# Kernel tuning notes

Hardware: AMD Instinct MI355X
Metric: run time of the kernel (lower is better)

## Reference

```python
import jax, jax.numpy as jnp
import numpy as np

IN_CAPS = 512
NUM_CAPS = 64
DIM_CAPS = 16
NUM_ROUTING = 3
BETA = 1.0  # config['Model']['temperature']
IN_DIM = 768
Q_N = 512
EPS = 1e-8


def squash(s):
    # capsule squash along last dim
    n2 = jnp.sum(s * s, axis=-1, keepdims=True)
    return (n2 / (1.0 + n2)) * s / jnp.sqrt(n2 + EPS)


def pearsonr(x, y):
    # pearson correlation along last dim, broadcasting leading dims
    xm = x - jnp.mean(x, axis=-1, keepdims=True)
    ym = y - jnp.mean(y, axis=-1, keepdims=True)
    num = jnp.sum(xm * ym, axis=-1)
    den = jnp.sqrt(jnp.sum(xm * xm, axis=-1) * jnp.sum(ym * ym, axis=-1) + EPS)
    return num / den


def setup_inputs() -> dict:
    key = jax.random.key(0)
    k1, k2, k3, k4 = jax.random.split(key, 4)
    m = jax.random.normal(k1, (IN_CAPS, IN_DIM), dtype=jnp.float32)
    q = jax.random.normal(k2, (Q_N, IN_DIM), dtype=jnp.float32)
    W_w = jax.random.normal(k3, (IN_DIM, NUM_CAPS * DIM_CAPS), dtype=jnp.float32) * 0.02
    W_b = jax.random.normal(k4, (NUM_CAPS * DIM_CAPS,), dtype=jnp.float32) * 0.02
    return {"m": m, "q": q, "W_w": W_w, "W_b": W_b}


def reference(m, q, W_w, W_b):
    nq = q.shape[0]
    hat_m = (m @ W_w + W_b).reshape(IN_CAPS, NUM_CAPS, DIM_CAPS)          # [I,C,D]
    hat_q = (q @ W_w + W_b).reshape(nq, NUM_CAPS, DIM_CAPS)               # [Q,C,D]

    m_sg = jax.lax.stop_gradient(hat_m)                                    # detached copies used in routing
    # torch expands hat_q along in_caps but updates it uniformly -> keep broadcast dim of size 1
    q_cur = jax.lax.stop_gradient(hat_q)[:, None, :, :]                    # [Q,1,C,D]

    a = jnp.zeros((nq, IN_CAPS, NUM_CAPS), dtype=hat_m.dtype)             # routing logits
    p = jnp.tanh(pearsonr(m_sg[None], q_cur))                              # [Q,I,C]

    for _ in range(NUM_ROUTING - 1):
        d = jax.nn.softmax(a / BETA, axis=2)                               # softmax over num_caps (as in torch dim=2)
        d_sum_p = d + p                                                     # [Q,I,C]
        hat_v = jnp.einsum('qic,icd->qcd', d_sum_p, m_sg)                  # sum over in_caps
        v = squash(hat_v)                                                   # [Q,C,D]
        hat_m_cos_v = jnp.einsum('icd,qcd->qic', m_sg, v)                  # [Q,I,C]
        a = a + p * hat_m_cos_v
        q_cur = (q_cur + v[:, None]) / 2.0                                  # stays [Q,1,C,D]
        p = jnp.tanh(pearsonr(m_sg[None], q_cur))

    d = jax.nn.softmax(a / BETA, axis=2)
    d_sum_p = jax.lax.stop_gradient(d + p)                                  # detached coefficients
    hat_v = jnp.einsum('qic,icd->qcd', d_sum_p, hat_m)                      # grad flows only through hat_m
    q_prime = squash(hat_v).reshape(nq, -1)                                 # [Q, C*D]
    return q_prime
```

## Files before the change

kernel.cpp:

```cpp
#include <hip/hip_runtime.h>
#include <math.h>

#define IN_CAPS 512
#define QN      512
#define IN_DIM  768
#define NCAPS   64
#define DCAPS   16
#define CD      1024

typedef _Float16 half2_t __attribute__((ext_vector_type(2)));

#if __has_builtin(__builtin_amdgcn_rcpf)
  #define RCP(x) __builtin_amdgcn_rcpf(x)
#else
  #define RCP(x) __frcp_rn(x)
#endif

__device__ __forceinline__ float tanh_pade(float x){
  const float x2 = x*x;
  const float num = fmaf(x2, x2 + 105.0f, 945.0f);
  const float den = fmaf(x2, fmaf(x2, 15.0f, 420.0f), 945.0f);
  return x * num * RCP(den);
}

template<int CTRL>
__device__ __forceinline__ float dpp_add(float v){
  int r = __builtin_amdgcn_update_dpp(0, __float_as_int(v), CTRL, 0xF, 0xF, true);
  return v + __int_as_float(r);
}

__device__ __forceinline__ float wave_sum64_all(float v){
  v = dpp_add<0xB1>(v);
  v = dpp_add<0x4E>(v);
  v = dpp_add<0x141>(v);
  v = dpp_add<0x140>(v);
  v = dpp_add<0x142>(v);
  v = dpp_add<0x143>(v);
  return __int_as_float(__builtin_amdgcn_readlane(__float_as_int(v), 63));
}

#define LD16(dst, ptr) { const float4* _p=(const float4*)(ptr); \
  float4 _a=_p[0], _b=_p[1], _c=_p[2], _d=_p[3]; \
  dst[0]=_a.x; dst[1]=_a.y; dst[2]=_a.z; dst[3]=_a.w; \
  dst[4]=_b.x; dst[5]=_b.y; dst[6]=_b.z; dst[7]=_b.w; \
  dst[8]=_c.x; dst[9]=_c.y; dst[10]=_c.z; dst[11]=_c.w; \
  dst[12]=_d.x; dst[13]=_d.y; dst[14]=_d.z; dst[15]=_d.w; }

#define ST16(ptr, src) { float4* _p=(float4*)(ptr); \
  _p[0]=make_float4(src[0],src[1],src[2],src[3]); \
  _p[1]=make_float4(src[4],src[5],src[6],src[7]); \
  _p[2]=make_float4(src[8],src[9],src[10],src[11]); \
  _p[3]=make_float4(src[12],src[13],src[14],src[15]); }

#define LDH(dst, ptrf4) { const float4* _p=(const float4*)(ptrf4); \
  float4 _a=_p[0], _b=_p[1]; \
  dst[0]=__builtin_bit_cast(half2_t,_a.x); dst[1]=__builtin_bit_cast(half2_t,_a.y); \
  dst[2]=__builtin_bit_cast(half2_t,_a.z); dst[3]=__builtin_bit_cast(half2_t,_a.w); \
  dst[4]=__builtin_bit_cast(half2_t,_b.x); dst[5]=__builtin_bit_cast(half2_t,_b.y); \
  dst[6]=__builtin_bit_cast(half2_t,_b.z); dst[7]=__builtin_bit_cast(half2_t,_b.w); }

#define CVT16(dst, h) { \
  _Pragma("unroll") for (int _j=0;_j<8;_j++){ \
    dst[2*_j]   = (float)h[_j].x; \
    dst[2*_j+1] = (float)h[_j].y; } }

#define STH16(ptr, src) { float _tb[8]; \
  _Pragma("unroll") for (int _j=0;_j<8;_j++){ half2_t _h; _h.x=(_Float16)src[2*_j]; _h.y=(_Float16)src[2*_j+1]; _tb[_j]=__builtin_bit_cast(float,_h);} \
  float4* _p=(float4*)(ptr); \
  _p[0]=make_float4(_tb[0],_tb[1],_tb[2],_tb[3]); \
  _p[1]=make_float4(_tb[4],_tb[5],_tb[6],_tb[7]); }

#define DOT16(res, x, y) { float _e=0.f,_o=0.f; \
  _Pragma("unroll") for (int _d=0;_d<16;_d+=2){ _e = fmaf(x[_d],y[_d],_e); _o = fmaf(x[_d+1],y[_d+1],_o); } \
  res = _e+_o; }

#define ACCUM(acc, m, w) { \
  _Pragma("unroll") for (int _d=0;_d<16;_d++) acc[_d] = fmaf(w, m[_d], acc[_d]); }

#define QSTAT(qcc, s1v, qq) { \
  float qc_[16]; \
  LD16(qc_, hat + (size_t)(IN_CAPS + (qq))*CD + c*16); \
  float s_=0.f; \
  _Pragma("unroll") for (int d=0;d<16;d++) s_ += qc_[d]; \
  const float mean_ = s_*(1.0f/16.0f); \
  float n2_=0.f; \
  _Pragma("unroll") for (int d=0;d<16;d++){ qcc[d]=qc_[d]-mean_; n2_ += qcc[d]*qcc[d]; } \
  s1v = __frsqrt_rn(n2_ + 1e-12f); }

#define WDECODE() \
  const int tid = threadIdx.x; \
  const int gw  = blockIdx.x*4 + (tid >> 6); \
  const int q   = gw >> cshift; \
  const int ch  = gw & (nch-1); \
  const int c   = tid & 63;

__global__ __launch_bounds__(256) void gemm_hat(const float* __restrict__ m,
                                                const float* __restrict__ q,
                                                const float* __restrict__ Ww,
                                                float* __restrict__ hatP)
{
  __shared__ float As[16][65];
  __shared__ float Bs[16][65];
  const int tid = threadIdx.x;
  const int bm = blockIdx.y, bn = blockIdx.x, kz = blockIdx.z;
  const int tx = tid & 15, ty = tid >> 4;

  float acc[4][4];
  #pragma unroll
  for (int a=0;a<4;a++)
    #pragma unroll
    for (int b=0;b<4;b++) acc[a][b]=0.0f;

  const int r  = tid >> 2;
  const int kk = (tid & 3) << 2;
  const int row = bm*64 + r;
  const float* srcA = (row < IN_CAPS) ? (m + row*IN_DIM) : (q + (row-IN_CAPS)*IN_DIM);
  const int krow = tid >> 4;
  const int cc   = (tid & 15) << 2;

  const int kbeg = kz*(IN_DIM/4), kend = kbeg + IN_DIM/4;
  for (int k0=kbeg; k0<kend; k0+=16){
    float4 av = *(const float4*)(srcA + k0 + kk);
    As[kk+0][r]=av.x; As[kk+1][r]=av.y; As[kk+2][r]=av.z; As[kk+3][r]=av.w;
    float4 bv = *(const float4*)(Ww + (size_t)(k0+krow)*CD + bn*64 + cc);
    Bs[krow][cc+0]=bv.x; Bs[krow][cc+1]=bv.y; Bs[krow][cc+2]=bv.z; Bs[krow][cc+3]=bv.w;
    __syncthreads();
    #pragma unroll
    for (int k=0;k<16;k++){
      float a[4], b[4];
      #pragma unroll
      for (int j=0;j<4;j++) a[j] = As[k][ty*4+j];
      #pragma unroll
      for (int j=0;j<4;j++) b[j] = Bs[k][tx*4+j];
      #pragma unroll
      for (int ii=0;ii<4;ii++)
        #pragma unroll
        for (int jj=0;jj<4;jj++) acc[ii][jj] += a[ii]*b[jj];
    }
    __syncthreads();
  }
  float* dst = hatP + (size_t)kz*1048576;
  const int col0 = bn*64 + tx*4;
  #pragma unroll
  for (int ii=0;ii<4;ii++){
    const int orow = bm*64 + ty*4 + ii;
    #pragma unroll
    for (int jj=0;jj<4;jj++) dst[(size_t)orow*CD + col0 + jj] = acc[ii][jj];
  }
}

__global__ __launch_bounds__(256) void finish_stats_kernel(const float4* __restrict__ hatP4,
                                                           const float* __restrict__ Wb,
                                                           float4* __restrict__ hat4,
                                                           _Float16* __restrict__ hatH,
                                                           float2* __restrict__ rs,
                                                           float* __restrict__ s1g,
                                                           _Float16* __restrict__ qccH)
{
  __shared__ float rowbuf[1024];
  const int row = blockIdx.x;
  const int t = threadIdx.x;
  const size_t o = (size_t)row*256 + t;
  float4 a = hatP4[o];
  float4 b = hatP4[o + 262144];
  float4 cx = hatP4[o + 524288];
  float4 d = hatP4[o + 786432];
  const float4 wb = *(const float4*)(Wb + t*4);
  float4 r;
  r.x = a.x+b.x+cx.x+d.x+wb.x;
  r.y = a.y+b.y+cx.y+d.y+wb.y;
  r.z = a.z+b.z+cx.z+d.z+wb.z;
  r.w = a.w+b.w+cx.w+d.w+wb.w;
  hat4[o] = r;
  if (row < IN_CAPS){
    half2_t h0, h1;
    h0.x=(_Float16)r.x; h0.y=(_Float16)r.y;
    h1.x=(_Float16)r.z; h1.y=(_Float16)r.w;
    *(float2*)(hatH + (size_t)row*CD + t*4) =
      make_float2(__builtin_bit_cast(float,h0), __builtin_bit_cast(float,h1));
  }
  rowbuf[t*4+0]=r.x; rowbuf[t*4+1]=r.y; rowbuf[t*4+2]=r.z; rowbuf[t*4+3]=r.w;
  __syncthreads();
  if (t < 64){
    const int c = t;
    float v[16];
    #pragma unroll
    for (int dd=0;dd<16;dd++) v[dd] = rowbuf[c*16+dd];
    float s=0.f;
    #pragma unroll
    for (int dd=0;dd<16;dd++) s += v[dd];
    const float mean = s*(1.0f/16.0f);
    float n2=0.f;
    #pragma unroll
    for (int dd=0;dd<16;dd++){ float x=v[dd]-mean; n2+=x*x; }
    if (row < IN_CAPS){
      rs[row*64+c] = make_float2(__frsqrt_rn(n2 + 1e-12f), s);
    } else {
      const int qr = row - IN_CAPS;
      s1g[qr*64 + c] = __frsqrt_rn(n2 + 1e-12f);
      float tbuf[8];
      #pragma unroll
      for (int j=0;j<8;j++){
        half2_t h; h.x=(_Float16)(v[2*j]-mean); h.y=(_Float16)(v[2*j+1]-mean);
        tbuf[j] = __builtin_bit_cast(float, h);
      }
      float4* dst = (float4*)(qccH + (size_t)qr*CD + c*16);
      dst[0] = make_float4(tbuf[0],tbuf[1],tbuf[2],tbuf[3]);
      dst[1] = make_float4(tbuf[4],tbuf[5],tbuf[6],tbuf[7]);
    }
  }
}

template<bool CACHED>
__global__ __launch_bounds__(256) void pass1_kernel(const float4* __restrict__ hatH4,
                                                    const float4* __restrict__ qccH4,
                                                    const float* __restrict__ s1g,
                                                    const float2* __restrict__ rs_g,
                                                    _Float16* __restrict__ part,
                                                    _Float16* __restrict__ n1h,
                                                    int ilen, int nch, int cshift)
{
  WDECODE();
  float qcc1[16];
  {
    half2_t qh[8];
    LDH(qh, qccH4 + (size_t)q*128 + c*2);
    CVT16(qcc1, qh);
  }
  const float s1 = s1g[q*64+c];

  float acc[16];
  #pragma unroll
  for (int d=0;d<16;d++) acc[d]=0.f;

  const int i0 = ch*ilen;
  const float4* mp = hatH4 + (size_t)i0*128 + c*2;
  const float2* rp = rs_g + i0*64 + c;
  size_t idx = ((size_t)q*512 + i0)*64 + c;
  for (int i=0;i<ilen;i+=2, mp+=256, rp+=128, idx+=128){
    half2_t ha[8], hb[8];
    LDH(ha, mp); LDH(hb, mp+128);
    float ma[16], mb[16];
    CVT16(ma, ha); CVT16(mb, hb);
    const float ra = rp[0].x, rb = rp[64].x;
    float nA, nB;
    DOT16(nA, ma, qcc1);
    DOT16(nB, mb, qcc1);
    if (CACHED){
      n1h[idx]    = (_Float16)nA;
      n1h[idx+64] = (_Float16)nB;
    }
    const float wA = 0.015625f + tanh_pade(nA*ra*s1);
    const float wB = 0.015625f + tanh_pade(nB*rb*s1);
    ACCUM(acc, ma, wA);
    ACCUM(acc, mb, wB);
  }
  STH16(part + (((size_t)(q<<cshift) + ch)*64 + c)*16, acc);
}

__global__ __launch_bounds__(256) void reduce1_kernel(const float* __restrict__ hat,
                                                      const _Float16* __restrict__ part,
                                                      float* __restrict__ v1g,
                                                      float2* __restrict__ aux1,
                                                      int nchunk)
{
  const int tid = threadIdx.x;
  const int q = blockIdx.x*4 + (tid>>6), c = tid & 63;
  float hv[16];
  #pragma unroll
  for (int d=0;d<16;d++) hv[d]=0.f;
  const _Float16* pp = part + ((size_t)q*nchunk*64 + c)*16;
  for (int ch=0; ch<nchunk; ch++, pp += 1024){
    half2_t th[8]; LDH(th, pp);
    float t[16]; CVT16(t, th);
    #pragma unroll
    for (int d=0;d<16;d++) hv[d]+=t[d];
  }
  float n2=0.f;
  #pragma unroll
  for (int d=0;d<16;d++) n2 += hv[d]*hv[d];
  const float sc = n2 / ((1.0f+n2)*sqrtf(n2+1e-8f));
  float v1[16]; float sv=0.f;
  #pragma unroll
  for (int d=0;d<16;d++){ v1[d]=hv[d]*sc; sv+=v1[d]; }
  ST16(v1g + ((size_t)q*64 + c)*16, v1);
  float qc[16]; LD16(qc, hat + (size_t)(IN_CAPS+q)*CD + c*16);
  float s=0.f, ss=0.f;
  #pragma unroll
  for (int d=0;d<16;d++){ const float t2 = 0.5f*(qc[d]+v1[d]); s+=t2; ss+=t2*t2; }
  const float mean = s*(1.0f/16.0f);
  aux1[q*64+c] = make_float2(__frsqrt_rn(ss - 16.0f*mean*mean + 1e-12f), sv*(1.0f/16.0f));
}

template<bool CACHED>
__global__ __launch_bounds__(256) void pass2_kernel(const float4* __restrict__ hatH4,
                                                    const float* __restrict__ hat,
                                                    const float2* __restrict__ rs_g,
                                                    const float* __restrict__ s1g,
                                                    const float* __restrict__ v1g,
                                                    const float2* __restrict__ aux1,
                                                    _Float16* __restrict__ part,
                                                    _Float16* __restrict__ n1h,
                                                    float* __restrict__ c2f,
                                                    int ilen, int nch, int cshift)
{
  WDECODE();
  float qcc1[16]; float s1;
  if (CACHED){
    s1 = s1g[q*64+c];
  } else {
    QSTAT(qcc1, s1, q);
  }
  float v1[16];
  LD16(v1, v1g + ((size_t)q*64 + c)*16);
  const float2 a1 = aux1[q*64+c];
  const float s2 = a1.x, mv1 = a1.y;

  float acc[16];
  #pragma unroll
  for (int d=0;d<16;d++) acc[d]=0.f;

  const int i0 = ch*ilen;
  const float4* mp = hatH4 + (size_t)i0*128 + c*2;
  const float2* rp = rs_g + i0*64 + c;
  size_t idx = ((size_t)q*512 + i0)*64 + c;
  for (int i=0;i<ilen;i+=2, mp+=256, rp+=128, idx+=128){
    half2_t ha[8], hb[8];
    LDH(ha, mp); LDH(hb, mp+128);
    float ma[16], mb[16];
    CVT16(ma, ha); CVT16(mb, hb);
    const float2 ra = rp[0], rb = rp[64];
    float n1A, n1B, cvA, cvB;
    if (CACHED){
      n1A = (float)n1h[idx];
      n1B = (float)n1h[idx+64];
    } else {
      DOT16(n1A, ma, qcc1);
      DOT16(n1B, mb, qcc1);
    }
    DOT16(cvA, ma, v1);
    DOT16(cvB, mb, v1);
    const float p1A = tanh_pade(n1A*ra.x*s1);
    const float n2A = 0.5f*(n1A + cvA - mv1*ra.y);
    const float p2A = tanh_pade(n2A*ra.x*s2);
    const float p1B = tanh_pade(n1B*rb.x*s1);
    const float n2B = 0.5f*(n1B + cvB - mv1*rb.y);
    const float p2B = tanh_pade(n2B*rb.x*s2);
    const float l1A = p1A*cvA;
    const float l1B = p1B*cvB;
    if (CACHED){
      half2_t cA; cA.x = (_Float16)l1A; cA.y = (_Float16)p2A;
      half2_t cB; cB.x = (_Float16)l1B; cB.y = (_Float16)p2B;
      c2f[idx]    = __builtin_bit_cast(float, cA);
      c2f[idx+64] = __builtin_bit_cast(float, cB);
      n1h[idx]    = (_Float16)n2A;
      n1h[idx+64] = (_Float16)n2B;
    }
    const float eA = __expf(l1A);
    const float eB = __expf(l1B);
    const float SA = wave_sum64_all(eA);
    const float SB = wave_sum64_all(eB);
    const float wA = eA*RCP(SA) + p2A;
    const float wB = eB*RCP(SB) + p2B;
    ACCUM(acc, ma, wA);
    ACCUM(acc, mb, wB);
  }
  STH16(part + (((size_t)(q<<cshift) + ch)*64 + c)*16, acc);
}

__global__ __launch_bounds__(256) void reduce2_kernel(const float* __restrict__ hat,
                                                      const _Float16* __restrict__ part,
                                                      const float* __restrict__ v1g,
                                                      float* __restrict__ v2g,
                                                      float2* __restrict__ aux2,
                                                      int nchunk)
{
  const int tid = threadIdx.x;
  const int q = blockIdx.x*4 + (tid>>6), c = tid & 63;
  float hv[16];
  #pragma unroll
  for (int d=0;d<16;d++) hv[d]=0.f;
  const _Float16* pp = part + ((size_t)q*nchunk*64 + c)*16;
  for (int ch=0; ch<nchunk; ch++, pp += 1024){
    half2_t th[8]; LDH(th, pp);
    float t[16]; CVT16(t, th);
    #pragma unroll
    for (int d=0;d<16;d++) hv[d]+=t[d];
  }
  float n2=0.f;
  #pragma unroll
  for (int d=0;d<16;d++) n2 += hv[d]*hv[d];
  const float sc = n2 / ((1.0f+n2)*sqrtf(n2+1e-8f));
  float v2[16]; float sv=0.f;
  #pragma unroll
  for (int d=0;d<16;d++){ v2[d]=hv[d]*sc; sv+=v2[d]; }
  ST16(v2g + ((size_t)q*64 + c)*16, v2);
  float qc[16];  LD16(qc, hat + (size_t)(IN_CAPS+q)*CD + c*16);
  float v1[16];  LD16(v1, v1g + ((size_t)q*64 + c)*16);
  float s=0.f, ss=0.f;
  #pragma unroll
  for (int d=0;d<16;d++){
    const float t3 = 0.25f*qc[d] + 0.25f*v1[d] + 0.5f*v2[d];
    s+=t3; ss+=t3*t3;
  }
  const float mean = s*(1.0f/16.0f);
  aux2[q*64+c] = make_float2(__frsqrt_rn(ss - 16.0f*mean*mean + 1e-12f), sv*(1.0f/16.0f));
}

template<bool CACHED>
__global__ __launch_bounds__(256) void pass3_kernel(const float4* __restrict__ hatH4,
                                                    const float* __restrict__ hat,
                                                    const float2* __restrict__ rs_g,
                                                    const float* __restrict__ v1g,
                                                    const float* __restrict__ v2g,
                                                    const float2* __restrict__ aux1,
                                                    const float2* __restrict__ aux2,
                                                    _Float16* __restrict__ part,
                                                    const _Float16* __restrict__ n1h,
                                                    const float* __restrict__ c2f,
                                                    int ilen, int nch, int cshift)
{
  WDECODE();
  float v2[16];
  LD16(v2, v2g + ((size_t)q*64 + c)*16);
  const float2 a2 = aux2[q*64+c];
  const float s3 = a2.x, mv2 = a2.y;

  float qcc1[16]; float s1=0.f, s2=0.f, mv1=0.f;
  float v1[16];
  if (!CACHED){
    QSTAT(qcc1, s1, q);
    LD16(v1, v1g + ((size_t)q*64 + c)*16);
    const float2 a1 = aux1[q*64+c];
    s2 = a1.x; mv1 = a1.y;
  }

  float acc[16];
  #pragma unroll
  for (int d=0;d<16;d++) acc[d]=0.f;

  const int i0 = ch*ilen;
  const float4* mp = hatH4 + (size_t)i0*128 + c*2;
  const float2* rp = rs_g + i0*64 + c;
  size_t idx = ((size_t)q*512 + i0)*64 + c;
  for (int i=0;i<ilen;i+=2, mp+=256, rp+=128, idx+=128){
    half2_t ha[8], hb[8];
    LDH(ha, mp); LDH(hb, mp+128);
    float ma[16], mb[16];
    CVT16(ma, ha); CVT16(mb, hb);
    const float2 ra = rp[0], rb = rp[64];
    float cwA, cwB;
    DOT16(cwA, ma, v2);
    DOT16(cwB, mb, v2);
    float l1A, p2A, n2A, l1B, p2B, n2B;
    if (CACHED){
      half2_t cA = __builtin_bit_cast(half2_t, c2f[idx]);
      half2_t cB = __builtin_bit_cast(half2_t, c2f[idx+64]);
      l1A = (float)cA.x; p2A = (float)cA.y;
      l1B = (float)cB.x; p2B = (float)cB.y;
      n2A = (float)n1h[idx];
      n2B = (float)n1h[idx+64];
    } else {
      float n1A, cvA, n1B, cvB;
      DOT16(n1A, ma, qcc1); DOT16(cvA, ma, v1);
      DOT16(n1B, mb, qcc1); DOT16(cvB, mb, v1);
      const float p1A = tanh_pade(n1A*ra.x*s1);
      n2A = 0.5f*(n1A + cvA - mv1*ra.y);
      p2A = tanh_pade(n2A*ra.x*s2);
      l1A = p1A*cvA;
      const float p1B = tanh_pade(n1B*rb.x*s1);
      n2B = 0.5f*(n1B + cvB - mv1*rb.y);
      p2B = tanh_pade(n2B*rb.x*s2);
      l1B = p1B*cvB;
    }
    const float n3A = 0.5f*(n2A + cwA - mv2*ra.y);
    const float p3A = tanh_pade(n3A*ra.x*s3);
    const float n3B = 0.5f*(n2B + cwB - mv2*rb.y);
    const float p3B = tanh_pade(n3B*rb.x*s3);
    const float eA = __expf(fmaf(p2A, cwA, l1A));
    const float eB = __expf(fmaf(p2B, cwB, l1B));
    const float SA = wave_sum64_all(eA);
    const float SB = wave_sum64_all(eB);
    const float wA = eA*RCP(SA) + p3A;
    const float wB = eB*RCP(SB) + p3B;
    ACCUM(acc, ma, wA);
    ACCUM(acc, mb, wB);
  }
  STH16(part + (((size_t)(q<<cshift) + ch)*64 + c)*16, acc);
}

__global__ __launch_bounds__(256) void reduce3_kernel(const _Float16* __restrict__ part,
                                                      float* __restrict__ out,
                                                      int nchunk)
{
  const int tid = threadIdx.x;
  const int q = blockIdx.x*4 + (tid>>6), c = tid & 63;
  float hv[16];
  #pragma unroll
  for (int d=0;d<16;d++) hv[d]=0.f;
  const _Float16* pp = part + ((size_t)q*nchunk*64 + c)*16;
  for (int ch=0; ch<nchunk; ch++, pp += 1024){
    half2_t th[8]; LDH(th, pp);
    float t[16]; CVT16(t, th);
    #pragma unroll
    for (int d=0;d<16;d++) hv[d]+=t[d];
  }
  float n2=0.f;
  #pragma unroll
  for (int d=0;d<16;d++) n2 += hv[d]*hv[d];
  const float sc = n2 / ((1.0f+n2)*sqrtf(n2+1e-8f));
  float o[16];
  #pragma unroll
  for (int d=0;d<16;d++) o[d] = hv[d]*sc;
  ST16(out + (size_t)q*CD + c*16, o);
}

extern "C" void kernel_launch(void* const* d_in, const int* in_sizes, int n_in,
                              void* d_out, int out_size, void* d_ws, size_t ws_size,
                              hipStream_t stream)
{
  const float* m  = (const float*)d_in[0];
  const float* q  = (const float*)d_in[1];
  const float* Ww = (const float*)d_in[2];
  const float* Wb = (const float*)d_in[3];
  float* out = (float*)d_out;

  char* ws = (char*)d_ws;
  float*    hat  = (float*)   (ws + 0);
  float2*   rs   = (float2*)  (ws + 4194304);
  _Float16* hatH = (_Float16*)(ws + 4456448);
  float*    s1g  = (float*)   (ws + 5505024);
  _Float16* qccH = (_Float16*)(ws + 5636096);
  float*    v1g  = (float*)   (ws + 6684672);
  float*    v2g  = (float*)   (ws + 8781824);
  float2*   aux1 = (float2*)  (ws + 10878976);
  float2*   aux2 = (float2*)  (ws + 11141120);
  const size_t base = 11403264ull;
  const size_t CACHE_BYTES = 33554432ull + 67108864ull;

  auto spanOf = [](int nc){ size_t s = (size_t)nc*1048576ull; return s < 16777216ull ? 16777216ull : s; };

  int nchunk = 16, cshift = 4;
  bool cached;
  {
    int nc = 16, cs = 4;
    while (nc > 1 && base + spanOf(nc) + CACHE_BYTES > ws_size){ nc >>= 1; cs--; }
    cached = (base + spanOf(nc) + CACHE_BYTES <= ws_size);
    if (cached){ nchunk = nc; cshift = cs; }
    else {
      while (nchunk > 1 && base + spanOf(nchunk) > ws_size){ nchunk >>= 1; cshift--; }
    }
  }
  const size_t span = spanOf(nchunk);
  _Float16* part = (_Float16*)(ws + base);
  float*    hatP = (float*)   (ws + base);
  _Float16* n1h  = (_Float16*)(ws + base + span);
  float*    c2f  = (float*)   (ws + base + span + 33554432ull);

  const int ilen = 512 / nchunk;
  const int pblocks = (QN*nchunk)/4;

  dim3 g0(16,16,4);
  gemm_hat<<<g0, 256, 0, stream>>>(m, q, Ww, hatP);
  finish_stats_kernel<<<1024, 256, 0, stream>>>((const float4*)hatP, Wb, (float4*)hat, hatH, rs, s1g, qccH);
  if (cached){
    pass1_kernel<true><<<pblocks, 256, 0, stream>>>((const float4*)hatH, (const float4*)qccH, s1g, rs, part, n1h, ilen, nchunk, cshift);
    reduce1_kernel<<<128, 256, 0, stream>>>(hat, part, v1g, aux1, nchunk);
    pass2_kernel<true><<<pblocks, 256, 0, stream>>>((const float4*)hatH, hat, rs, s1g, v1g, aux1, part, n1h, c2f, ilen, nchunk, cshift);
    reduce2_kernel<<<128, 256, 0, stream>>>(hat, part, v1g, v2g, aux2, nchunk);
    pass3_kernel<true><<<pblocks, 256, 0, stream>>>((const float4*)hatH, hat, rs, v1g, v2g, aux1, aux2, part, n1h, c2f, ilen, nchunk, cshift);
    reduce3_kernel<<<128, 256, 0, stream>>>(part, out, nchunk);
  } else {
    pass1_kernel<false><<<pblocks, 256, 0, stream>>>((const float4*)hatH, (const float4*)qccH, s1g, rs, part, n1h, ilen, nchunk, cshift);
    reduce1_kernel<<<128, 256, 0, stream>>>(hat, part, v1g, aux1, nchunk);
    pass2_kernel<false><<<pblocks, 256, 0, stream>>>((const float4*)hatH, hat, rs, s1g, v1g, aux1, part, n1h, c2f, ilen, nchunk, cshift);
    reduce2_kernel<<<128, 256, 0, stream>>>(hat, part, v1g, v2g, aux2, nchunk);
    pass3_kernel<false><<<pblocks, 256, 0, stream>>>((const float4*)hatH, hat, rs, v1g, v2g, aux1, aux2, part, n1h, c2f, ilen, nchunk, cshift);
    reduce3_kernel<<<128, 256, 0, stream>>>(part, out, nchunk);
  }
}
```

Measured before the change: 196.8 us.

## Process two queries per wave in routing passes to reuse capsule loads

Adds pass1/2/3 variants where each wave handles a pair of queries, so every loaded hat_m row (fp16) and its stats are reused for two queries. This halves the grid size and the global reads of the in-capsule tensor in the cached path. In exchange it doubles the live registers (two accumulators and two query vectors), which may lower occupancy, and halves the number of blocks available for parallelism.

```diff
diff --git a/kernel.cpp b/kernel.cpp
--- a/kernel.cpp
+++ b/kernel.cpp
@@ -92,6 +92,14 @@
   const int gw  = blockIdx.x*4 + (tid >> 6); \
   const int q   = gw >> cshift; \
   const int ch  = gw & (nch-1); \
+  const int c   = tid & 63;
+
+#define WDECODE2() \
+  const int tid = threadIdx.x; \
+  const int gw  = blockIdx.x*4 + (tid >> 6); \
+  const int qp  = gw >> cshift; \
+  const int ch  = gw & (nch-1); \
+  const int q0  = qp*2, q1 = q0+1; \
   const int c   = tid & 63;
 
 __global__ __launch_bounds__(256) void gemm_hat(const float* __restrict__ m,
@@ -210,6 +218,177 @@
     }
   }
 }
+
+
+__global__ __launch_bounds__(256) void pass1_q2(const float4* __restrict__ hatH4,
+                                                const float4* __restrict__ qccH4,
+                                                const float* __restrict__ s1g,
+                                                const float2* __restrict__ rs_g,
+                                                _Float16* __restrict__ part,
+                                                _Float16* __restrict__ n1h,
+                                                int ilen, int nch, int cshift)
+{
+  WDECODE2();
+  float qccA[16], qccB[16];
+  { half2_t qh[8]; LDH(qh, qccH4 + (size_t)q0*128 + c*2); CVT16(qccA, qh); }
+  { half2_t qh[8]; LDH(qh, qccH4 + (size_t)q1*128 + c*2); CVT16(qccB, qh); }
+  const float s1A = s1g[q0*64+c], s1B = s1g[q1*64+c];
+
+  float accA[16], accB[16];
+  #pragma unroll
+  for (int d=0;d<16;d++){ accA[d]=0.f; accB[d]=0.f; }
+
+  const int i0 = ch*ilen;
+  const float4* mp = hatH4 + (size_t)i0*128 + c*2;
+  const float2* rp = rs_g + i0*64 + c;
+  size_t idxA = ((size_t)q0*512 + i0)*64 + c;
+  size_t idxB = idxA + 32768;
+  for (int i=0;i<ilen;i++, mp+=128, rp+=64, idxA+=64, idxB+=64){
+    half2_t h[8];
+    LDH(h, mp);
+    float mr[16];
+    CVT16(mr, h);
+    const float rn = rp->x;
+    float nA, nB;
+    DOT16(nA, mr, qccA);
+    DOT16(nB, mr, qccB);
+    n1h[idxA] = (_Float16)nA;
+    n1h[idxB] = (_Float16)nB;
+    const float wA = 0.015625f + tanh_pade(nA*rn*s1A);
+    const float wB = 0.015625f + tanh_pade(nB*rn*s1B);
+    ACCUM(accA, mr, wA);
+    ACCUM(accB, mr, wB);
+  }
+  STH16(part + (((size_t)(q0<<cshift) + ch)*64 + c)*16, accA);
+  STH16(part + (((size_t)(q1<<cshift) + ch)*64 + c)*16, accB);
+}
+
+__global__ __launch_bounds__(256) void pass2_q2(const float4* __restrict__ hatH4,
+                                                const float2* __restrict__ rs_g,
+                                                const float* __restrict__ s1g,
+                                                const float* __restrict__ v1g,
+                                                const float2* __restrict__ aux1,
+                                                _Float16* __restrict__ part,
+                                                _Float16* __restrict__ n1h,
+                                                float* __restrict__ c2f,
+                                                int ilen, int nch, int cshift)
+{
+  WDECODE2();
+  const float s1A = s1g[q0*64+c], s1B = s1g[q1*64+c];
+  float v1A[16], v1B[16];
+  LD16(v1A, v1g + ((size_t)q0*64 + c)*16);
+  LD16(v1B, v1g + ((size_t)q1*64 + c)*16);
+  const float2 a1A = aux1[q0*64+c];
+  const float2 a1B = aux1[q1*64+c];
+  const float s2A = a1A.x, mv1A = a1A.y;
+  const float s2B = a1B.x, mv1B = a1B.y;
+
+  float accA[16], accB[16];
+  #pragma unroll
+  for (int d=0;d<16;d++){ accA[d]=0.f; accB[d]=0.f; }
+
+  const int i0 = ch*ilen;
+  const float4* mp = hatH4 + (size_t)i0*128 + c*2;
+  const float2* rp = rs_g + i0*64 + c;
+  size_t idxA = ((size_t)q0*512 + i0)*64 + c;
+  size_t idxB = idxA + 32768;
+  for (int i=0;i<ilen;i++, mp+=128, rp+=64, idxA+=64, idxB+=64){
+    half2_t h[8];
+    LDH(h, mp);
+    float mr[16];
+    CVT16(mr, h);
+    const float2 rn = *rp;
+    const float n1A = (float)n1h[idxA];
+    const float n1B = (float)n1h[idxB];
+    float cvA, cvB;
+    DOT16(cvA, mr, v1A);
+    DOT16(cvB, mr, v1B);
+    const float p1A = tanh_pade(n1A*rn.x*s1A);
+    const float n2A = 0.5f*(n1A + cvA - mv1A*rn.y);
+    const float p2A = tanh_pade(n2A*rn.x*s2A);
+    const float p1B = tanh_pade(n1B*rn.x*s1B);
+    const float n2B = 0.5f*(n1B + cvB - mv1B*rn.y);
+    const float p2B = tanh_pade(n2B*rn.x*s2B);
+    const float l1A = p1A*cvA;
+    const float l1B = p1B*cvB;
+    half2_t cA; cA.x = (_Float16)l1A; cA.y = (_Float16)p2A;
+    half2_t cB; cB.x = (_Float16)l1B; cB.y = (_Float16)p2B;
+    c2f[idxA] = __builtin_bit_cast(float, cA);
+    c2f[idxB] = __builtin_bit_cast(float, cB);
+    n1h[idxA] = (_Float16)n2A;
+    n1h[idxB] = (_Float16)n2B;
+    const float eA = __expf(l1A);
+    const float eB = __expf(l1B);
+    const float SA = wave_sum64_all(eA);
+    const float SB = wave_sum64_all(eB);
+    const float wA = eA*RCP(SA) + p2A;
+    const float wB = eB*RCP(SB) + p2B;
+    ACCUM(accA, mr, wA);
+    ACCUM(accB, mr, wB);
+  }
+  STH16(part + (((size_t)(q0<<cshift) + ch)*64 + c)*16, accA);
+  STH16(part + (((size_t)(q1<<cshift) + ch)*64 + c)*16, accB);
+}
+
+__global__ __launch_bounds__(256) void pass3_q2(const float4* __restrict__ hatH4,
+                                                const float2* __restrict__ rs_g,
+                                                const float* __restrict__ v2g,
+                                                const float2* __restrict__ aux2,
+                                                _Float16* __restrict__ part,
+                                                const _Float16* __restrict__ n1h,
+                                                const float* __restrict__ c2f,
+                                                int ilen, int nch, int cshift)
+{
+  WDECODE2();
+  float v2A[16], v2B[16];
+  LD16(v2A, v2g + ((size_t)q0*64 + c)*16);
+  LD16(v2B, v2g + ((size_t)q1*64 + c)*16);
+  const float2 a2A = aux2[q0*64+c];
+  const float2 a2B = aux2[q1*64+c];
+  const float s3A = a2A.x, mv2A = a2A.y;
+  const float s3B = a2B.x, mv2B = a2B.y;
+
+  float accA[16], accB[16];
+  #pragma unroll
+  for (int d=0;d<16;d++){ accA[d]=0.f; accB[d]=0.f; }
+
+  const int i0 = ch*ilen;
+  const float4* mp = hatH4 + (size_t)i0*128 + c*2;
+  const float2* rp = rs_g + i0*64 + c;
+  size_t idxA = ((size_t)q0*512 + i0)*64 + c;
+  size_t idxB = idxA + 32768;
+  for (int i=0;i<ilen;i++, mp+=128, rp+=64, idxA+=64, idxB+=64){
+    half2_t h[8];
+    LDH(h, mp);
+    float mr[16];
+    CVT16(mr, h);
+    const float2 rn = *rp;
+    float cwA, cwB;
+    DOT16(cwA, mr, v2A);
+    DOT16(cwB, mr, v2B);
+    half2_t cA = __builtin_bit_cast(half2_t, c2f[idxA]);
+    half2_t cB = __builtin_bit_cast(half2_t, c2f[idxB]);
+    const float l1A = (float)cA.x, p2A = (float)cA.y;
+    const float l1B = (float)cB.x, p2B = (float)cB.y;
+    const float n2A = (float)n1h[idxA];
+    const float n2B = (float)n1h[idxB];
+    const float n3A = 0.5f*(n2A + cwA - mv2A*rn.y);
+    const float p3A = tanh_pade(n3A*rn.x*s3A);
+    const float n3B = 0.5f*(n2B + cwB - mv2B*rn.y);
+    const float p3B = tanh_pade(n3B*rn.x*s3B);
+    const float eA = __expf(fmaf(p2A, cwA, l1A));
+    const float eB = __expf(fmaf(p2B, cwB, l1B));
+    const float SA = wave_sum64_all(eA);
+    const float SB = wave_sum64_all(eB);
+    const float wA = eA*RCP(SA) + p3A;
+    const float wB = eB*RCP(SB) + p3B;
+    ACCUM(accA, mr, wA);
+    ACCUM(accB, mr, wB);
+  }
+  STH16(part + (((size_t)(q0<<cshift) + ch)*64 + c)*16, accA);
+  STH16(part + (((size_t)(q1<<cshift) + ch)*64 + c)*16, accB);
+}
+
 
 template<bool CACHED>
 __global__ __launch_bounds__(256) void pass1_kernel(const float4* __restrict__ hatH4,
@@ -558,17 +737,18 @@
   float*    c2f  = (float*)   (ws + base + span + 33554432ull);
 
   const int ilen = 512 / nchunk;
-  const int pblocks = (QN*nchunk)/4;
+  const int pblocks  = (QN*nchunk)/4;
+  const int pblocks2 = (QN/2*nchunk)/4;
 
   dim3 g0(16,16,4);
   gemm_hat<<<g0, 256, 0, stream>>>(m, q, Ww, hatP);
   finish_stats_kernel<<<1024, 256, 0, stream>>>((const float4*)hatP, Wb, (float4*)hat, hatH, rs, s1g, qccH);
   if (cached){
-    pass1_kernel<true><<<pblocks, 256, 0, stream>>>((const float4*)hatH, (const float4*)qccH, s1g, rs, part, n1h, ilen, nchunk, cshift);
+    pass1_q2<<<pblocks2, 256, 0, stream>>>((const float4*)hatH, (const float4*)qccH, s1g, rs, part, n1h, ilen, nchunk, cshift);
     reduce1_kernel<<<128, 256, 0, stream>>>(hat, part, v1g, aux1, nchunk);
-    pass2_kernel<true><<<pblocks, 256, 0, stream>>>((const float4*)hatH, hat, rs, s1g, v1g, aux1, part, n1h, c2f, ilen, nchunk, cshift);
+    pass2_q2<<<pblocks2, 256, 0, stream>>>((const float4*)hatH, rs, s1g, v1g, aux1, part, n1h, c2f, ilen, nchunk, cshift);
     reduce2_kernel<<<128, 256, 0, stream>>>(hat, part, v1g, v2g, aux2, nchunk);
-    pass3_kernel<true><<<pblocks, 256, 0, stream>>>((const float4*)hatH, hat, rs, v1g, v2g, aux1, aux2, part, n1h, c2f, ilen, nchunk, cshift);
+    pass3_q2<<<pblocks2, 256, 0, stream>>>((const float4*)hatH, rs, v2g, aux2, part, n1h, c2f, ilen, nchunk, cshift);
     reduce3_kernel<<<128, 256, 0, stream>>>(part, out, nchunk);
   } else {
     pass1_kernel<false><<<pblocks, 256, 0, stream>>>((const float4*)hatH, (const float4*)qccH, s1g, rs, part, n1h, ilen, nchunk, cshift);
```

Result: faster. 183.8 us (-6.6%).
